# Kernel tuning notes

Hardware: AMD Instinct MI355X
Metric: run time of the kernel (lower is better)

## Reference

```python
import jax, jax.numpy as jnp
import numpy as np

N, E, DIN, HID, H, ED = 50000, 800000, 128, 64, 4, 5
Z_IDX = 3          # impedance column
PHYS_W = 1.0       # physics_weight
NEG_SLOPE = 0.2    # GATv2 leaky_relu slope


def gat_layer(x, src, dst, ea, Wl, bl, Wr, br, We, att, temp, bias, concat):
    """PhysicsGATv2Conv (add_self_loops=False, eval mode / no dropout)."""
    n = x.shape[0]
    Hh, C = att.shape
    xl = (x @ Wl + bl).reshape(n, Hh, C)   # lin_l -> source features
    xr = (x @ Wr + br).reshape(n, Hh, C)   # lin_r -> target features
    # physics-enhanced edge attr: overwrite last column with temp * w / |Z|
    z = jnp.clip(ea[:, Z_IDX], 1e-6, None)
    ea = ea.at[:, -1].set(temp * PHYS_W / z)
    e = (ea @ We).reshape(-1, Hh, C)       # lin_edge (no bias)
    m = jax.nn.leaky_relu(xl[src] + xr[dst] + e, NEG_SLOPE)  # [E,H,C]
    logit = jnp.einsum('ehc,hc->eh', m, att)                 # [E,H]
    # segment softmax over incoming edges of each target node
    lmax = jax.ops.segment_max(logit, dst, num_segments=n)
    w = jnp.exp(logit - lmax[dst])
    den = jax.ops.segment_sum(w, dst, num_segments=n)
    a = w / (den[dst] + 1e-16)
    out = jax.ops.segment_sum(xl[src] * a[:, :, None], dst, num_segments=n)
    out = out.reshape(n, Hh * C) if concat else out.mean(axis=1)
    return out + bias


def layer_norm(x, w, b):
    mu = x.mean(-1, keepdims=True)
    v = ((x - mu) ** 2).mean(-1, keepdims=True)
    return (x - mu) * jax.lax.rsqrt(v + 1e-5) * w + b


def setup_inputs() -> dict:
    key = jax.random.key(0)
    ks = iter(jax.random.split(key, 40))
    nk = lambda: next(ks)
    d = {}
    d['x'] = jax.random.normal(nk(), (N, DIN), jnp.float32)
    d['edge_index'] = jax.random.randint(nk(), (2, E), 0, N)
    d['edge_attr'] = jax.random.uniform(nk(), (E, ED), jnp.float32)
    hd = HID * H
    cfg = [(DIN, True), (hd, True), (hd, False)]
    for i, (din, concat) in enumerate(cfg):
        dout = hd if concat else HID
        d[f'Wl{i}'] = jax.random.normal(nk(), (din, hd), jnp.float32) / np.sqrt(din)
        d[f'bl{i}'] = 0.01 * jax.random.normal(nk(), (hd,), jnp.float32)
        d[f'Wr{i}'] = jax.random.normal(nk(), (din, hd), jnp.float32) / np.sqrt(din)
        d[f'br{i}'] = 0.01 * jax.random.normal(nk(), (hd,), jnp.float32)
        d[f'We{i}'] = jax.random.normal(nk(), (ED, hd), jnp.float32) / np.sqrt(ED)
        d[f'att{i}'] = jax.random.normal(nk(), (H, HID), jnp.float32) / np.sqrt(HID)
        d[f'temp{i}'] = jnp.float32(1.0)
        d[f'bias{i}'] = 0.01 * jax.random.normal(nk(), (dout,), jnp.float32)
        d[f'lnw{i}'] = jnp.ones((dout,), jnp.float32)
        d[f'lnb{i}'] = jnp.zeros((dout,), jnp.float32)
    d['pw0'] = jax.random.normal(nk(), (DIN, hd), jnp.float32) / np.sqrt(DIN)
    d['pb0'] = jnp.zeros((hd,), jnp.float32)
    d['pw2'] = jax.random.normal(nk(), (hd, HID), jnp.float32) / np.sqrt(hd)
    d['pb2'] = jnp.zeros((HID,), jnp.float32)
    return d


def reference(x, edge_index, edge_attr,
              Wl0, bl0, Wr0, br0, We0, att0, temp0, bias0, lnw0, lnb0,
              Wl1, bl1, Wr1, br1, We1, att1, temp1, bias1, lnw1, lnb1,
              Wl2, bl2, Wr2, br2, We2, att2, temp2, bias2, lnw2, lnb2,
              pw0, pb0, pw2, pb2):
    src, dst = edge_index[0], edge_index[1]
    # layer 0: 128 -> 256 (concat), residual projected
    h = gat_layer(x, src, dst, edge_attr, Wl0, bl0, Wr0, br0, We0, att0, temp0, bias0, True)
    h = layer_norm(h, lnw0, lnb0) + (x @ pw0 + pb0)
    h = jax.nn.elu(h)
    # layer 1: 256 -> 256 (concat), identity residual
    h1 = gat_layer(h, src, dst, edge_attr, Wl1, bl1, Wr1, br1, We1, att1, temp1, bias1, True)
    h = layer_norm(h1, lnw1, lnb1) + h
    h = jax.nn.elu(h)
    # layer 2: 256 -> 64 (head-mean), residual projected, no activation
    h2 = gat_layer(h, src, dst, edge_attr, Wl2, bl2, Wr2, br2, We2, att2, temp2, bias2, False)
    out = layer_norm(h2, lnw2, lnb2) + (h @ pw2 + pb2)
    return out
```

## Files before the change

### kernel.cpp

```cpp
#include <hip/hip_runtime.h>
#include <math.h>

#define NN 50000
#define EE 800000
#define NB 196

typedef _Float16 half8 __attribute__((ext_vector_type(8)));
typedef _Float16 hv4  __attribute__((ext_vector_type(4)));
typedef float floatx16 __attribute__((ext_vector_type(16)));
typedef float fv4 __attribute__((ext_vector_type(4)));

template<int CTRL>
__device__ __forceinline__ float dppadd(float x) {
    int t = __builtin_amdgcn_update_dpp(0, __float_as_int(x), CTRL, 0xf, 0xf, false);
    return x + __int_as_float(t);
}
__device__ __forceinline__ float red16(float x) {
    x = dppadd<0x121>(x);
    x = dppadd<0x122>(x);
    x = dppadd<0x124>(x);
    x = dppadd<0x128>(x);
    return x;
}

__global__ __launch_bounds__(256) void swizzleA(
    const float* __restrict__ A, _Float16* __restrict__ Asw, int M, int K)
{
    int wave = threadIdx.x >> 6, lane = threadIdx.x & 63;
    int tile = blockIdx.x;
    int kc = blockIdx.y * 4 + wave;
    int KC = K >> 4;
    int row = tile * 32 + (lane & 31);
    int k0 = kc * 16 + (lane >> 5) * 8;
    float4 v0 = make_float4(0.f, 0.f, 0.f, 0.f);
    float4 v1 = make_float4(0.f, 0.f, 0.f, 0.f);
    if (row < M) {
        const float* p = A + (size_t)row * K + k0;
        v0 = *(const float4*)p;
        v1 = *(const float4*)(p + 4);
    }
    half8 o;
    o[0] = (_Float16)v0.x; o[1] = (_Float16)v0.y;
    o[2] = (_Float16)v0.z; o[3] = (_Float16)v0.w;
    o[4] = (_Float16)v1.x; o[5] = (_Float16)v1.y;
    o[6] = (_Float16)v1.z; o[7] = (_Float16)v1.w;
    *(half8*)(Asw + (((size_t)tile * KC + kc) * 64 + lane) * 8) = o;
}

__global__ __launch_bounds__(256) void swizzleB(
    const float* __restrict__ B, _Float16* __restrict__ Bsw, int K, int NC)
{
    int wave = threadIdx.x >> 6, lane = threadIdx.x & 63;
    int KC = K >> 4, NT = NC >> 5;
    int pair = blockIdx.x * 4 + wave;
    if (pair >= NT * KC) return;
    int nt = pair / KC, kc = pair - nt * KC;
    int n = nt * 32 + (lane & 31);
    int k0 = kc * 16 + (lane >> 5) * 8;
    half8 o;
#pragma unroll
    for (int j = 0; j < 8; ++j)
        o[j] = (_Float16)B[(size_t)(k0 + j) * NC + n];
    *(half8*)(Bsw + ((size_t)pair * 64 + lane) * 8) = o;
}

__global__ __launch_bounds__(256) void cat3(
    const float* __restrict__ b0, int n0, const float* __restrict__ b1, int n1,
    const float* __restrict__ b2, int n2, float* __restrict__ out)
{
    int i = blockIdx.x * 256 + threadIdx.x;
    if (i < n0) out[i] = b0[i];
    else if (i < n0 + n1) out[i] = b1[i - n0];
    else if (i < n0 + n1 + n2) out[i] = b2[i - n0 - n1];
}

template<int CT, typename OT>
__global__ __launch_bounds__(256) void gemm_mfma(
    const _Float16* __restrict__ Asw, const _Float16* __restrict__ Bsw,
    const float* __restrict__ bias, OT* __restrict__ C,
    int M, int K, int NC)
{
    const int wave = threadIdx.x >> 6, lane = threadIdx.x & 63;
    const int KC = K >> 4;
    const int rt0 = blockIdx.x * 4 + (wave & 1) * 2;
    const int ct0 = blockIdx.y * (2 * CT) + (wave >> 1) * CT;

    const half8* Ap0 = (const half8*)Asw + (size_t)rt0 * KC * 64 + lane;
    const half8* Ap1 = Ap0 + (size_t)KC * 64;
    const half8* Bp0 = (const half8*)Bsw + (size_t)ct0 * KC * 64 + lane;
    const half8* Bp1 = Bp0 + (size_t)KC * 64;

    floatx16 acc00 = {0.f}, acc10 = {0.f}, acc01 = {0.f}, acc11 = {0.f};

    for (int kc = 0; kc < KC; ++kc) {
        half8 a0 = Ap0[(size_t)kc * 64];
        half8 a1 = Ap1[(size_t)kc * 64];
        half8 b0 = Bp0[(size_t)kc * 64];
        acc00 = __builtin_amdgcn_mfma_f32_32x32x16_f16(a0, b0, acc00, 0, 0, 0);
        acc10 = __builtin_amdgcn_mfma_f32_32x32x16_f16(a1, b0, acc10, 0, 0, 0);
        if (CT == 2) {
            half8 b1 = Bp1[(size_t)kc * 64];
            acc01 = __builtin_amdgcn_mfma_f32_32x32x16_f16(a0, b1, acc01, 0, 0, 0);
            acc11 = __builtin_amdgcn_mfma_f32_32x32x16_f16(a1, b1, acc11, 0, 0, 0);
        }
    }

    const int nlane = lane & 31, hs = lane >> 5;
#pragma unroll
    for (int c = 0; c < CT; ++c) {
        int col = (ct0 + c) * 32 + nlane;
        float bb = bias[col];
        const floatx16& a_ = (c == 0) ? acc00 : acc01;
        const floatx16& b_ = (c == 0) ? acc10 : acc11;
#pragma unroll
        for (int r = 0; r < 16; ++r) {
            int rowin = (r & 3) + 8 * (r >> 2) + 4 * hs;
            int row0 = rt0 * 32 + rowin;
            int row1 = row0 + 32;
            if (row0 < M) C[(size_t)row0 * NC + col] = (OT)(a_[r] + bb);
            if (row1 < M) C[(size_t)row1 * NC + col] = (OT)(b_[r] + bb);
        }
    }
}

__global__ __launch_bounds__(256) void hist_kernel(const int* __restrict__ dst,
                                                   int* __restrict__ deg)
{
    int e = blockIdx.x * 256 + threadIdx.x;
    if (e < EE) atomicAdd(&deg[dst[e]], 1);
}

__global__ __launch_bounds__(256) void scan_local(const int* __restrict__ deg,
                                                  int* __restrict__ rowoff,
                                                  int* __restrict__ part)
{
    __shared__ int sd[256];
    int tid = threadIdx.x;
    int i = blockIdx.x * 256 + tid;
    int v = (i < NN) ? deg[i] : 0;
    sd[tid] = v;
    __syncthreads();
    for (int off = 1; off < 256; off <<= 1) {
        int t = (tid >= off) ? sd[tid - off] : 0;
        __syncthreads();
        sd[tid] += t;
        __syncthreads();
    }
    if (i < NN) rowoff[i] = sd[tid] - v;
    if (tid == 255) part[blockIdx.x] = sd[255];
}

__global__ __launch_bounds__(256) void scan_part(int* __restrict__ part,
                                                 int* __restrict__ rowoff)
{
    __shared__ int sd[256];
    int tid = threadIdx.x;
    int v = (tid < NB) ? part[tid] : 0;
    sd[tid] = v;
    __syncthreads();
    for (int off = 1; off < 256; off <<= 1) {
        int t = (tid >= off) ? sd[tid - off] : 0;
        __syncthreads();
        sd[tid] += t;
        __syncthreads();
    }
    if (tid < NB) part[tid] = sd[tid] - v;
    if (tid == 0) rowoff[NN] = EE;
}

__global__ __launch_bounds__(256) void scan_add(int* __restrict__ rowoff,
                                                const int* __restrict__ part)
{
    int i = blockIdx.x * 256 + threadIdx.x;
    if (i < NN) rowoff[i] += part[blockIdx.x];
}

__global__ __launch_bounds__(256) void scatter_kernel(
    const int* __restrict__ src, const int* __restrict__ dst,
    const float* __restrict__ ea, const int* __restrict__ rowoff,
    int* __restrict__ cursor, int* __restrict__ srcp,
    float4* __restrict__ eap, float* __restrict__ erec)
{
    int e = blockIdx.x * 256 + threadIdx.x;
    if (e < EE) {
        int d = dst[e];
        int pos = rowoff[d] + atomicAdd(&cursor[d], 1);
        srcp[pos] = src[e];
        const float* p = ea + (size_t)e * 5;
        eap[pos] = make_float4(p[0], p[1], p[2], p[3]);
        erec[pos] = 1.0f / fmaxf(p[3], 1e-6f);
    }
}

__global__ __launch_bounds__(256) void fused_attn_ln(
    const int* __restrict__ rowoff, const int* __restrict__ srcp,
    const float4* __restrict__ eap, const float* __restrict__ erec,
    const _Float16* __restrict__ xlp, int rstride,
    const float* __restrict__ We, const float* __restrict__ att,
    const float* __restrict__ temp, const float* __restrict__ bias,
    const float* __restrict__ lnw, const float* __restrict__ lnb,
    const _Float16* __restrict__ residH, const float* __restrict__ residF,
    float* __restrict__ out, int mode)
{
    int v = __builtin_amdgcn_readfirstlane(blockIdx.x * 4 + (threadIdx.x >> 6));
    int lane = threadIdx.x & 63;
    if (v >= NN) return;
    int grp = lane >> 4;
    int sub = lane & 15;
    int j = grp * 64 + sub * 4;

    fv4 ww0 = *(const fv4*)(We + j);
    fv4 ww1 = *(const fv4*)(We + 256 + j);
    fv4 ww2 = *(const fv4*)(We + 512 + j);
    fv4 ww3 = *(const fv4*)(We + 768 + j);
    fv4 ww4 = *(const fv4*)(We + 1024 + j);
    fv4 atv = *(const fv4*)(att + j);
    fv4 xrv = __builtin_convertvector(
        *(const hv4*)(xlp + (size_t)v * rstride + 256 + j), fv4);
    float tmp = temp[0];
    const float L2E = 1.44269504088896340736f;

    float mxd = -INFINITY, dend = 0.f;
    fv4 acc = {0.f, 0.f, 0.f, 0.f};

    int beg = rowoff[v], end = rowoff[v + 1];
    int i = beg;
    for (; i + 2 <= end; i += 2) {
        int s0 = srcp[i], s1 = srcp[i + 1];
        float4 a0 = eap[i], a1 = eap[i + 1];
        float q0 = tmp * erec[i], q1 = tmp * erec[i + 1];
        fv4 x0 = __builtin_convertvector(
            *(const hv4*)(xlp + (size_t)s0 * rstride + j), fv4);
        fv4 x1 = __builtin_convertvector(
            *(const hv4*)(xlp + (size_t)s1 * rstride + j), fv4);
        fv4 m0 = x0 + xrv;
        m0 = m0 + a0.x * ww0; m0 = m0 + a0.y * ww1; m0 = m0 + a0.z * ww2;
        m0 = m0 + a0.w * ww3; m0 = m0 + q0 * ww4;
        fv4 m1 = x1 + xrv;
        m1 = m1 + a1.x * ww0; m1 = m1 + a1.y * ww1; m1 = m1 + a1.z * ww2;
        m1 = m1 + a1.w * ww3; m1 = m1 + q1 * ww4;
        m0 = __builtin_elementwise_max(m0, m0 * 0.2f);
        m1 = __builtin_elementwise_max(m1, m1 * 0.2f);
        fv4 p0 = m0 * atv, p1 = m1 * atv;
        float l0 = (p0[0] + p0[1]) + (p0[2] + p0[3]);
        float l1 = (p1[0] + p1[1]) + (p1[2] + p1[3]);
        l0 = red16(l0) * L2E;
        l1 = red16(l1) * L2E;
        float nm = fmaxf(mxd, fmaxf(l0, l1));
        float sc = exp2f(mxd - nm);
        float e0 = exp2f(l0 - nm);
        float e1 = exp2f(l1 - nm);
        mxd = nm;
        dend = dend * sc + (e0 + e1);
        acc = acc * sc + (x0 * e0 + x1 * e1);
    }
    if (i < end) {
        int s0 = srcp[i];
        float4 a0 = eap[i];
        float q0 = tmp * erec[i];
        fv4 x0 = __builtin_convertvector(
            *(const hv4*)(xlp + (size_t)s0 * rstride + j), fv4);
        fv4 m0 = x0 + xrv;
        m0 = m0 + a0.x * ww0; m0 = m0 + a0.y * ww1; m0 = m0 + a0.z * ww2;
        m0 = m0 + a0.w * ww3; m0 = m0 + q0 * ww4;
        m0 = __builtin_elementwise_max(m0, m0 * 0.2f);
        fv4 p0 = m0 * atv;
        float l0 = (p0[0] + p0[1]) + (p0[2] + p0[3]);
        l0 = red16(l0) * L2E;
        float nm = fmaxf(mxd, l0);
        float sc = exp2f(mxd - nm);
        float e0 = exp2f(l0 - nm);
        mxd = nm;
        dend = dend * sc + e0;
        acc = acc * sc + x0 * e0;
    }

    float inv = 1.f / (dend + 1e-16f);
    if (mode <= 1) {
        fv4 bb = *(const fv4*)(bias + j);
        fv4 o = acc * inv + bb;
        float s  = (o[0] + o[1]) + (o[2] + o[3]);
        fv4 oq = o * o;
        float s2 = (oq[0] + oq[1]) + (oq[2] + oq[3]);
        s = red16(s);   s += __shfl_xor(s, 16, 64);  s += __shfl_xor(s, 32, 64);
        s2 = red16(s2); s2 += __shfl_xor(s2, 16, 64); s2 += __shfl_xor(s2, 32, 64);
        float mu = s * (1.f / 256.f);
        float var = s2 * (1.f / 256.f) - mu * mu;
        float rs = rsqrtf(var + 1e-5f);
        fv4 lw = *(const fv4*)(lnw + j);
        fv4 lb = *(const fv4*)(lnb + j);
        fv4 rr;
        if (mode == 0)
            rr = __builtin_convertvector(
                *(const hv4*)(residH + (size_t)v * rstride + j), fv4);
        else
            rr = *(const fv4*)(residF + (size_t)v * 256 + j);
        fv4 y = (o - mu) * rs * lw + lb + rr;
        y[0] = (y[0] > 0.f) ? y[0] : expm1f(y[0]);
        y[1] = (y[1] > 0.f) ? y[1] : expm1f(y[1]);
        y[2] = (y[2] > 0.f) ? y[2] : expm1f(y[2]);
        y[3] = (y[3] > 0.f) ? y[3] : expm1f(y[3]);
        *(fv4*)(out + (size_t)v * 256 + j) = y;
    } else {
        fv4 r = acc * inv;
        r[0] += __shfl_xor(r[0], 16, 64); r[0] += __shfl_xor(r[0], 32, 64);
        r[1] += __shfl_xor(r[1], 16, 64); r[1] += __shfl_xor(r[1], 32, 64);
        r[2] += __shfl_xor(r[2], 16, 64); r[2] += __shfl_xor(r[2], 32, 64);
        r[3] += __shfl_xor(r[3], 16, 64); r[3] += __shfl_xor(r[3], 32, 64);
        fv4 bb = *(const fv4*)(bias + sub * 4);
        fv4 o = r * 0.25f + bb;
        float s  = (o[0] + o[1]) + (o[2] + o[3]);
        fv4 oq = o * o;
        float s2 = (oq[0] + oq[1]) + (oq[2] + oq[3]);
        s = red16(s);
        s2 = red16(s2);
        float mu = s * (1.f / 64.f);
        float var = s2 * (1.f / 64.f) - mu * mu;
        float rs = rsqrtf(var + 1e-5f);
        fv4 lw = *(const fv4*)(lnw + sub * 4);
        fv4 lb = *(const fv4*)(lnb + sub * 4);
        fv4 rr = *(const fv4*)(residF + (size_t)v * 64 + sub * 4);
        fv4 y = (o - mu) * rs * lw + lb + rr;
        if (grp == 0)
            *(fv4*)(out + (size_t)v * 64 + sub * 4) = y;
    }
}

extern "C" void kernel_launch(void* const* d_in, const int* in_sizes, int n_in,
                              void* d_out, int out_size, void* d_ws, size_t ws_size,
                              hipStream_t stream)
{
    const float* x    = (const float*)d_in[0];
    const int*   eidx = (const int*)d_in[1];
    const float* ea   = (const float*)d_in[2];
    const int* src = eidx;
    const int* dst = eidx + EE;

    const float *Wl[3], *bl[3], *Wr[3], *br[3], *We[3], *att[3], *temp[3],
                *bias[3], *lnw[3], *lnb[3];
    for (int i = 0; i < 3; ++i) {
        int b = 3 + i * 10;
        Wl[i]   = (const float*)d_in[b + 0];
        bl[i]   = (const float*)d_in[b + 1];
        Wr[i]   = (const float*)d_in[b + 2];
        br[i]   = (const float*)d_in[b + 3];
        We[i]   = (const float*)d_in[b + 4];
        att[i]  = (const float*)d_in[b + 5];
        temp[i] = (const float*)d_in[b + 6];
        bias[i] = (const float*)d_in[b + 7];
        lnw[i]  = (const float*)d_in[b + 8];
        lnb[i]  = (const float*)d_in[b + 9];
    }
    const float* pw0 = (const float*)d_in[33];
    const float* pb0 = (const float*)d_in[34];
    const float* pw2 = (const float*)d_in[35];
    const float* pb2 = (const float*)d_in[36];

    char* w = (char*)d_ws;
    float* h     = (float*)w; w += (size_t)NN * 256 * 4;
    char*  gbase = w;         w += (size_t)NN * 256 * 4;
    _Float16* xlr = (_Float16*)w; w += (size_t)NN * 768 * 2;
    float4* eap  = (float4*)w; w += (size_t)EE * 16;
    float* erec  = (float*)w; w += (size_t)EE * 4;
    int* srcp    = (int*)w;   w += (size_t)EE * 4;
    int* rowoff  = (int*)w;   w += (size_t)(NN + 16) * 4;
    int* cursor  = (int*)w;   w += (size_t)NN * 4;
    int* part    = (int*)w;   w += 1024;
    w = (char*)(((uintptr_t)w + 255) & ~(uintptr_t)255);
    _Float16* catB0 = (_Float16*)w; w += 196608;
    _Float16* catB1 = (_Float16*)w; w += 262144;
    _Float16* catB2 = (_Float16*)w; w += 262144;
    _Float16* B3    = (_Float16*)w; w += 32768;
    float* cb0 = (float*)w; w += 768 * 4;
    float* cb1 = (float*)w; w += 512 * 4;
    float* cb2 = (float*)w; w += 512 * 4;
    _Float16* Asw = (_Float16*)gbase;
    float* r64 = (float*)(gbase + (size_t)32 * 1024 * 1024);

    dim3 blk(256);
    dim3 grid_e((EE + 255) / 256);
    dim3 grid_nw((NN + 3) / 4);
    dim3 grid_nb(NB);
    const int MT = 391;

    auto swA = [&](const float* A, int K) {
        swizzleA<<<dim3(4 * MT, (K >> 4) / 4), blk, 0, stream>>>(A, Asw, NN, K);
    };
    auto swB = [&](const float* B, _Float16* dest, int K, int NC) {
        int pairs = (NC >> 5) * (K >> 4);
        swizzleB<<<dim3((pairs + 3) / 4), blk, 0, stream>>>(B, dest, K, NC);
    };
    auto attn = [&](int L, int rstride, const _Float16* residH,
                    const float* residF, float* outp, int mode) {
        fused_attn_ln<<<grid_nw, blk, 0, stream>>>(
            rowoff, srcp, eap, erec, xlr, rstride, We[L], att[L], temp[L],
            bias[L], lnw[L], lnb[L], residH, residF, outp, mode);
    };

    hipMemsetAsync(cursor, 0, (size_t)NN * 4, stream);
    hipLaunchKernelGGL(hist_kernel, grid_e, blk, 0, stream, dst, cursor);
    hipLaunchKernelGGL(scan_local, grid_nb, blk, 0, stream, cursor, rowoff, part);
    hipLaunchKernelGGL(scan_part, dim3(1), blk, 0, stream, part, rowoff);
    hipLaunchKernelGGL(scan_add, grid_nb, blk, 0, stream, rowoff, part);
    hipMemsetAsync(cursor, 0, (size_t)NN * 4, stream);
    hipLaunchKernelGGL(scatter_kernel, grid_e, blk, 0, stream,
                       src, dst, ea, rowoff, cursor, srcp, eap, erec);

    swB(Wl[0], catB0,              128, 256);
    swB(Wr[0], catB0 + 8 * 4096,   128, 256);
    swB(pw0,   catB0 + 16 * 4096,  128, 256);
    swB(Wl[1], catB1,              256, 256);
    swB(Wr[1], catB1 + 8 * 8192,   256, 256);
    swB(Wl[2], catB2,              256, 256);
    swB(Wr[2], catB2 + 8 * 8192,   256, 256);
    swB(pw2,   B3,                 256, 64);
    cat3<<<dim3(3), blk, 0, stream>>>(bl[0], 256, br[0], 256, pb0, 256, cb0);
    cat3<<<dim3(2), blk, 0, stream>>>(bl[1], 256, br[1], 256, nullptr, 0, cb1);
    cat3<<<dim3(2), blk, 0, stream>>>(bl[2], 256, br[2], 256, nullptr, 0, cb2);

    swA(x, 128);
    gemm_mfma<2, _Float16><<<dim3(MT, 6), blk, 0, stream>>>(
        Asw, catB0, cb0, xlr, NN, 128, 768);
    attn(0, 768, xlr + 512, nullptr, h, 0);

    swA(h, 256);
    gemm_mfma<2, _Float16><<<dim3(MT, 4), blk, 0, stream>>>(
        Asw, catB1, cb1, xlr, NN, 256, 512);
    attn(1, 512, nullptr, h, h, 1);

    swA(h, 256);
    gemm_mfma<2, _Float16><<<dim3(MT, 4), blk, 0, stream>>>(
        Asw, catB2, cb2, xlr, NN, 256, 512);
    gemm_mfma<1, float><<<dim3(MT, 1), blk, 0, stream>>>(
        Asw, B3, pb2, r64, NN, 256, 64);
    attn(2, 512, nullptr, r64, (float*)d_out, 2);
}
```

Baseline: 768.0 us.

## Fuse A-swizzle into attention epilogue, merge weight prep, use fast intrinsics

The attention+LayerNorm kernel now writes its fp16 output directly in the swizzled MFMA A-layout, which removes two swizzleA passes over the 50000x256 activations. The pw2 residual GEMM output moves into the fp16 xlr buffer with stride 576. The eight weight-swizzle launches and three bias-concat launches are merged into one prep kernel, and the second cursor memset is folded into scan_add. exp2, reciprocal, rsqrt and expm1 now use hardware approximate intrinsics, trading some precision (ELU via exp2 minus one, fp16 residual) for fewer instructions.

```diff
diff --git a/kernel.cpp b/kernel.cpp
--- a/kernel.cpp
+++ b/kernel.cpp
@@ -9,6 +9,8 @@
 typedef _Float16 hv4  __attribute__((ext_vector_type(4)));
 typedef float floatx16 __attribute__((ext_vector_type(16)));
 typedef float fv4 __attribute__((ext_vector_type(4)));
+
+__device__ __forceinline__ float fexp2(float x) { return __builtin_amdgcn_exp2f(x); }
 
 template<int CTRL>
 __device__ __forceinline__ float dppadd(float x) {
@@ -47,37 +49,61 @@
     *(half8*)(Asw + (((size_t)tile * KC + kc) * 64 + lane) * 8) = o;
 }
 
-__global__ __launch_bounds__(256) void swizzleB(
-    const float* __restrict__ B, _Float16* __restrict__ Bsw, int K, int NC)
-{
+__global__ __launch_bounds__(256) void prep_weights(
+    const float* __restrict__ s0, const float* __restrict__ s1,
+    const float* __restrict__ s2, const float* __restrict__ s3,
+    const float* __restrict__ s4, const float* __restrict__ s5,
+    const float* __restrict__ s6, const float* __restrict__ s7,
+    _Float16* __restrict__ catB0, _Float16* __restrict__ catB1,
+    _Float16* __restrict__ catB2,
+    const float* __restrict__ bl0, const float* __restrict__ br0,
+    const float* __restrict__ pb0, const float* __restrict__ bl1,
+    const float* __restrict__ br1, const float* __restrict__ bl2,
+    const float* __restrict__ br2, const float* __restrict__ pb2,
+    float* __restrict__ cb0, float* __restrict__ cb1, float* __restrict__ cb2)
+{
+    int b = blockIdx.x;
+    if (b >= 184) {
+        int t = (b - 184) * 256 + threadIdx.x;
+        if (t < 768) {
+            cb0[t] = (t < 256) ? bl0[t] : (t < 512) ? br0[t - 256] : pb0[t - 512];
+        } else if (t < 1280) {
+            int u = t - 768;
+            cb1[u] = (u < 256) ? bl1[u] : br1[u - 256];
+        } else if (t < 1856) {
+            int u = t - 1280;
+            cb2[u] = (u < 256) ? bl2[u] : (u < 512) ? br2[u - 256] : pb2[u - 512];
+        }
+        return;
+    }
     int wave = threadIdx.x >> 6, lane = threadIdx.x & 63;
-    int KC = K >> 4, NT = NC >> 5;
-    int pair = blockIdx.x * 4 + wave;
-    if (pair >= NT * KC) return;
-    int nt = pair / KC, kc = pair - nt * KC;
+    int pair = b * 4 + wave;
+    const int cum[9] = {0, 64, 128, 192, 320, 448, 576, 704, 736};
+    int job = 0;
+    while (pair >= cum[job + 1]) ++job;
+    const float* srcs[8] = {s0, s1, s2, s3, s4, s5, s6, s7};
+    const int KCs[8] = {8, 8, 8, 16, 16, 16, 16, 16};
+    const int NCs[8] = {256, 256, 256, 256, 256, 256, 256, 64};
+    const int ntb[8] = {0, 8, 16, 0, 8, 0, 8, 16};
+    _Float16* dsts[8] = {catB0, catB0, catB0, catB1, catB1, catB2, catB2, catB2};
+    int p = pair - cum[job];
+    int KC = KCs[job], NC = NCs[job];
+    int nt = p / KC, kc = p - nt * KC;
     int n = nt * 32 + (lane & 31);
     int k0 = kc * 16 + (lane >> 5) * 8;
+    const float* B = srcs[job];
     half8 o;
 #pragma unroll
-    for (int j = 0; j < 8; ++j)
-        o[j] = (_Float16)B[(size_t)(k0 + j) * NC + n];
-    *(half8*)(Bsw + ((size_t)pair * 64 + lane) * 8) = o;
-}
-
-__global__ __launch_bounds__(256) void cat3(
-    const float* __restrict__ b0, int n0, const float* __restrict__ b1, int n1,
-    const float* __restrict__ b2, int n2, float* __restrict__ out)
-{
-    int i = blockIdx.x * 256 + threadIdx.x;
-    if (i < n0) out[i] = b0[i];
-    else if (i < n0 + n1) out[i] = b1[i - n0];
-    else if (i < n0 + n1 + n2) out[i] = b2[i - n0 - n1];
-}
-
-template<int CT, typename OT>
+    for (int jj = 0; jj < 8; ++jj)
+        o[jj] = (_Float16)B[(size_t)(k0 + jj) * NC + n];
+    int ntG = ntb[job] + nt;
+    *(half8*)(dsts[job] + (((size_t)ntG * KC + kc) * 64 + lane) * 8) = o;
+}
+
+template<int CT>
 __global__ __launch_bounds__(256) void gemm_mfma(
     const _Float16* __restrict__ Asw, const _Float16* __restrict__ Bsw,
-    const float* __restrict__ bias, OT* __restrict__ C,
+    const float* __restrict__ bias, _Float16* __restrict__ C,
     int M, int K, int NC)
 {
     const int wave = threadIdx.x >> 6, lane = threadIdx.x & 63;
@@ -117,8 +143,8 @@
             int rowin = (r & 3) + 8 * (r >> 2) + 4 * hs;
             int row0 = rt0 * 32 + rowin;
             int row1 = row0 + 32;
-            if (row0 < M) C[(size_t)row0 * NC + col] = (OT)(a_[r] + bb);
-            if (row1 < M) C[(size_t)row1 * NC + col] = (OT)(b_[r] + bb);
+            if (row0 < M) C[(size_t)row0 * NC + col] = (_Float16)(a_[r] + bb);
+            if (row1 < M) C[(size_t)row1 * NC + col] = (_Float16)(b_[r] + bb);
         }
     }
 }
@@ -169,10 +195,14 @@
 }
 
 __global__ __launch_bounds__(256) void scan_add(int* __restrict__ rowoff,
-                                                const int* __restrict__ part)
+                                                const int* __restrict__ part,
+                                                int* __restrict__ cursor)
 {
     int i = blockIdx.x * 256 + threadIdx.x;
-    if (i < NN) rowoff[i] += part[blockIdx.x];
+    if (i < NN) {
+        rowoff[i] += part[blockIdx.x];
+        cursor[i] = 0;
+    }
 }
 
 __global__ __launch_bounds__(256) void scatter_kernel(
@@ -200,7 +230,7 @@
     const float* __restrict__ temp, const float* __restrict__ bias,
     const float* __restrict__ lnw, const float* __restrict__ lnb,
     const _Float16* __restrict__ residH, const float* __restrict__ residF,
-    float* __restrict__ out, int mode)
+    float* __restrict__ outF, _Float16* __restrict__ aswOut, int mode)
 {
     int v = __builtin_amdgcn_readfirstlane(blockIdx.x * 4 + (threadIdx.x >> 6));
     int lane = threadIdx.x & 63;
@@ -247,9 +277,9 @@
         l0 = red16(l0) * L2E;
         l1 = red16(l1) * L2E;
         float nm = fmaxf(mxd, fmaxf(l0, l1));
-        float sc = exp2f(mxd - nm);
-        float e0 = exp2f(l0 - nm);
-        float e1 = exp2f(l1 - nm);
+        float sc = fexp2(mxd - nm);
+        float e0 = fexp2(l0 - nm);
+        float e1 = fexp2(l1 - nm);
         mxd = nm;
         dend = dend * sc + (e0 + e1);
         acc = acc * sc + (x0 * e0 + x1 * e1);
@@ -268,14 +298,14 @@
         float l0 = (p0[0] + p0[1]) + (p0[2] + p0[3]);
         l0 = red16(l0) * L2E;
         float nm = fmaxf(mxd, l0);
-        float sc = exp2f(mxd - nm);
-        float e0 = exp2f(l0 - nm);
+        float sc = fexp2(mxd - nm);
+        float e0 = fexp2(l0 - nm);
         mxd = nm;
         dend = dend * sc + e0;
         acc = acc * sc + x0 * e0;
     }
 
-    float inv = 1.f / (dend + 1e-16f);
+    float inv = __builtin_amdgcn_rcpf(dend + 1e-16f);
     if (mode <= 1) {
         fv4 bb = *(const fv4*)(bias + j);
         fv4 o = acc * inv + bb;
@@ -286,7 +316,7 @@
         s2 = red16(s2); s2 += __shfl_xor(s2, 16, 64); s2 += __shfl_xor(s2, 32, 64);
         float mu = s * (1.f / 256.f);
         float var = s2 * (1.f / 256.f) - mu * mu;
-        float rs = rsqrtf(var + 1e-5f);
+        float rs = __builtin_amdgcn_rsqf(var + 1e-5f);
         fv4 lw = *(const fv4*)(lnw + j);
         fv4 lb = *(const fv4*)(lnb + j);
         fv4 rr;
@@ -296,11 +326,16 @@
         else
             rr = *(const fv4*)(residF + (size_t)v * 256 + j);
         fv4 y = (o - mu) * rs * lw + lb + rr;
-        y[0] = (y[0] > 0.f) ? y[0] : expm1f(y[0]);
-        y[1] = (y[1] > 0.f) ? y[1] : expm1f(y[1]);
-        y[2] = (y[2] > 0.f) ? y[2] : expm1f(y[2]);
-        y[3] = (y[3] > 0.f) ? y[3] : expm1f(y[3]);
-        *(fv4*)(out + (size_t)v * 256 + j) = y;
+        y[0] = (y[0] > 0.f) ? y[0] : fexp2(y[0] * L2E) - 1.f;
+        y[1] = (y[1] > 0.f) ? y[1] : fexp2(y[1] * L2E) - 1.f;
+        y[2] = (y[2] > 0.f) ? y[2] : fexp2(y[2] * L2E) - 1.f;
+        y[3] = (y[3] > 0.f) ? y[3] : fexp2(y[3] * L2E) - 1.f;
+        if (mode == 0)
+            *(fv4*)(outF + (size_t)v * 256 + j) = y;
+        int kc = j >> 4, half = (j >> 3) & 1, off = j & 7;
+        size_t idx = (((size_t)(v >> 5) * 16 + kc) * 64 + (v & 31) + 32 * half) * 8 + off;
+        hv4 yh = __builtin_convertvector(y, hv4);
+        *(hv4*)(aswOut + idx) = yh;
     } else {
         fv4 r = acc * inv;
         r[0] += __shfl_xor(r[0], 16, 64); r[0] += __shfl_xor(r[0], 32, 64);
@@ -316,13 +351,14 @@
         s2 = red16(s2);
         float mu = s * (1.f / 64.f);
         float var = s2 * (1.f / 64.f) - mu * mu;
-        float rs = rsqrtf(var + 1e-5f);
+        float rs = __builtin_amdgcn_rsqf(var + 1e-5f);
         fv4 lw = *(const fv4*)(lnw + sub * 4);
         fv4 lb = *(const fv4*)(lnb + sub * 4);
-        fv4 rr = *(const fv4*)(residF + (size_t)v * 64 + sub * 4);
+        fv4 rr = __builtin_convertvector(
+            *(const hv4*)(residH + (size_t)v * rstride + sub * 4), fv4);
         fv4 y = (o - mu) * rs * lw + lb + rr;
         if (grp == 0)
-            *(fv4*)(out + (size_t)v * 64 + sub * 4) = y;
+            *(fv4*)(outF + (size_t)v * 64 + sub * 4) = y;
     }
 }
 
@@ -369,13 +405,11 @@
     w = (char*)(((uintptr_t)w + 255) & ~(uintptr_t)255);
     _Float16* catB0 = (_Float16*)w; w += 196608;
     _Float16* catB1 = (_Float16*)w; w += 262144;
-    _Float16* catB2 = (_Float16*)w; w += 262144;
-    _Float16* B3    = (_Float16*)w; w += 32768;
+    _Float16* catB2 = (_Float16*)w; w += 294912;
     float* cb0 = (float*)w; w += 768 * 4;
     float* cb1 = (float*)w; w += 512 * 4;
-    float* cb2 = (float*)w; w += 512 * 4;
+    float* cb2 = (float*)w; w += 576 * 4;
     _Float16* Asw = (_Float16*)gbase;
-    float* r64 = (float*)(gbase + (size_t)32 * 1024 * 1024);
 
     dim3 blk(256);
     dim3 grid_e((EE + 255) / 256);
@@ -383,55 +417,39 @@
     dim3 grid_nb(NB);
     const int MT = 391;
 
-    auto swA = [&](const float* A, int K) {
-        swizzleA<<<dim3(4 * MT, (K >> 4) / 4), blk, 0, stream>>>(A, Asw, NN, K);
-    };
-    auto swB = [&](const float* B, _Float16* dest, int K, int NC) {
-        int pairs = (NC >> 5) * (K >> 4);
-        swizzleB<<<dim3((pairs + 3) / 4), blk, 0, stream>>>(B, dest, K, NC);
-    };
     auto attn = [&](int L, int rstride, const _Float16* residH,
-                    const float* residF, float* outp, int mode) {
+                    const float* residF, float* outFp, _Float16* asw, int mode) {
         fused_attn_ln<<<grid_nw, blk, 0, stream>>>(
             rowoff, srcp, eap, erec, xlr, rstride, We[L], att[L], temp[L],
-            bias[L], lnw[L], lnb[L], residH, residF, outp, mode);
+            bias[L], lnw[L], lnb[L], residH, residF, outFp, asw, mode);
     };
 
     hipMemsetAsync(cursor, 0, (size_t)NN * 4, stream);
     hipLaunchKernelGGL(hist_kernel, grid_e, blk, 0, stream, dst, cursor);
     hipLaunchKernelGGL(scan_local, grid_nb, blk, 0, stream, cursor, rowoff, part);
     hipLaunchKernelGGL(scan_part, dim3(1), blk, 0, stream, part, rowoff);
-    hipLaunchKernelGGL(scan_add, grid_nb, blk, 0, stream, rowoff, part);
-    hipMemsetAsync(cursor, 0, (size_t)NN * 4, stream);
+    hipLaunchKernelGGL(scan_add, grid_nb, blk, 0, stream, rowoff, part, cursor);
     hipLaunchKernelGGL(scatter_kernel, grid_e, blk, 0, stream,
                        src, dst, ea, rowoff, cursor, srcp, eap, erec);
 
-    swB(Wl[0], catB0,              128, 256);
-    swB(Wr[0], catB0 + 8 * 4096,   128, 256);
-    swB(pw0,   catB0 + 16 * 4096,  128, 256);
-    swB(Wl[1], catB1,              256, 256);
-    swB(Wr[1], catB1 + 8 * 8192,   256, 256);
-    swB(Wl[2], catB2,              256, 256);
-    swB(Wr[2], catB2 + 8 * 8192,   256, 256);
-    swB(pw2,   B3,                 256, 64);
-    cat3<<<dim3(3), blk, 0, stream>>>(bl[0], 256, br[0], 256, pb0, 256, cb0);
-    cat3<<<dim3(2), blk, 0, stream>>>(bl[1], 256, br[1], 256, nullptr, 0, cb1);
-    cat3<<<dim3(2), blk, 0, stream>>>(bl[2], 256, br[2], 256, nullptr, 0, cb2);
-
-    swA(x, 128);
-    gemm_mfma<2, _Float16><<<dim3(MT, 6), blk, 0, stream>>>(
+    hipLaunchKernelGGL(prep_weights, dim3(192), blk, 0, stream,
+                       Wl[0], Wr[0], pw0, Wl[1], Wr[1], Wl[2], Wr[2], pw2,
+                       catB0, catB1, catB2,
+                       bl[0], br[0], pb0, bl[1], br[1], bl[2], br[2], pb2,
+                       cb0, cb1, cb2);
+
+    swizzleA<<<dim3(4 * MT, 2), blk, 0, stream>>>(x, Asw, NN, 128);
+    gemm_mfma<2><<<dim3(MT, 6), blk, 0, stream>>>(
         Asw, catB0, cb0, xlr, NN, 128, 768);
-    attn(0, 768, xlr + 512, nullptr, h, 0);
-
-    swA(h, 256);
-    gemm_mfma<2, _Float16><<<dim3(MT, 4), blk, 0, stream>>>(
+    attn(0, 768, xlr + 512, nullptr, h, Asw, 0);
+
+    gemm_mfma<2><<<dim3(MT, 4), blk, 0, stream>>>(
         Asw, catB1, cb1, xlr, NN, 256, 512);
-    attn(1, 512, nullptr, h, h, 1);
-
-    swA(h, 256);
-    gemm_mfma<2, _Float16><<<dim3(MT, 4), blk, 0, stream>>>(
-        Asw, catB2, cb2, xlr, NN, 256, 512);
-    gemm_mfma<1, float><<<dim3(MT, 1), blk, 0, stream>>>(
-        Asw, B3, pb2, r64, NN, 256, 64);
-    attn(2, 512, nullptr, r64, (float*)d_out, 2);
-}
+    attn(1, 512, nullptr, h, nullptr, Asw, 1);
+
+    gemm_mfma<2><<<dim3(MT, 4), blk, 0, stream>>>(
+        Asw, catB2, cb2, xlr, NN, 256, 576);
+    gemm_mfma<1><<<dim3(MT, 1), blk, 0, stream>>>(
+        Asw, catB2 + 131072, cb2 + 512, xlr + 512, NN, 256, 576);
+    attn(2, 576, xlr + 512, nullptr, (float*)d_out, nullptr, 2);
+}
```

New measurement: 707.4 us. 7.9% less time.
